# Kernel tuning notes

Hardware: AMD Instinct MI355X
Metric: run time of the kernel (lower is better)

The kernel has to match this reference:

```python
import jax, jax.numpy as jnp
from jax import lax
import numpy as np

EPS_START, EPS_END, EPS_DECAY = 1.0, 0.05, 10000.0


def gru_step(x, h, w_ih, w_hh, b_ih, b_hh):
    # PyTorch GRUCell math; gates stacked as [r, z, n]
    gi = x @ w_ih.T + b_ih
    gh = h @ w_hh.T + b_hh
    i_r, i_z, i_n = jnp.split(gi, 3, axis=1)
    h_r, h_z, h_n = jnp.split(gh, 3, axis=1)
    r = jax.nn.sigmoid(i_r + h_r)
    z = jax.nn.sigmoid(i_z + h_z)
    n = jnp.tanh(i_n + r * h_n)
    return (1.0 - z) * n + z * h


def setup_inputs() -> dict:
    key = jax.random.key(0)
    ks = jax.random.split(key, 7)
    V, E, H = 32000, 256, 512
    s = 0.05
    return {
        "embedding": jax.random.normal(ks[0], (V, E), jnp.float32) * s,
        "w_ih": jax.random.normal(ks[1], (3 * H, E), jnp.float32) * s,
        "w_hh": jax.random.normal(ks[2], (3 * H, H), jnp.float32) * s,
        "b_ih": jax.random.normal(ks[3], (3 * H,), jnp.float32) * s,
        "b_hh": jax.random.normal(ks[4], (3 * H,), jnp.float32) * s,
        "w_out": jax.random.normal(ks[5], (V, H), jnp.float32) * s,
        "b_out": jax.random.normal(ks[6], (V,), jnp.float32) * s,
        "seq_len": 256,
        "batch_size": 512,
    }


def reference(embedding, w_ih, w_hh, b_ih, b_hh, w_out, b_out, seq_len, batch_size):
    V, E = embedding.shape
    H = w_hh.shape[1]
    B = batch_size
    log_unif = jnp.float32(np.log(V))  # -log(vocab_size) fill for epsilon-greedy

    keys = jax.random.split(jax.random.key(42), seq_len)
    ts = jnp.arange(seq_len, dtype=jnp.float32)

    h0 = jnp.zeros((B, H), jnp.float32)
    x0 = jnp.broadcast_to(embedding[0], (B, E))  # start token id 0

    def step(carry, inp):
        h, x = carry
        t, k = inp
        k_eps, k_gum = jax.random.split(k)
        h = gru_step(x, h, w_ih, w_hh, b_ih, b_hh)
        logp = jax.nn.log_softmax(h @ w_out.T + b_out, axis=1)  # [B, V]
        eps_t = EPS_END + (EPS_START - EPS_END) * jnp.exp(-4.0 * t / EPS_DECAY)
        draw = eps_t >= jax.random.uniform(k_eps, (B,))
        masked = jnp.where(draw[:, None], -log_unif, logp)
        g = jax.random.gumbel(k_gum, (B, V), jnp.float32)
        sampled = jnp.argmax(masked + g, axis=1)  # [B] int
        lp = jnp.take_along_axis(logp, sampled[:, None], axis=1)[:, 0]
        x_next = embedding[sampled]
        return (h, x_next), (sampled, lp)

    _, (samples, lps) = lax.scan(step, (h0, x0), (ts, keys))
    return samples.T, lps.T  # [B, S] each
```

## Files before the change

### kernel.cpp

```cpp
#include <hip/hip_runtime.h>
#include <math.h>
#include <stdio.h>

#ifndef JAX_PARTITIONABLE
#define JAX_PARTITIONABLE 1
#endif

namespace {

constexpr int B  = 512;
constexpr int S  = 256;
constexpr int E  = 256;
constexpr int H  = 512;
constexpr int V  = 32000;
constexpr int G3 = 3 * H;
constexpr int VBLK = 64;
constexpr int BBLK = 256;
constexpr int NCH  = V / VBLK;
constexpr int NDMAX = 96;

typedef __bf16 bf16x8 __attribute__((ext_vector_type(8)));
typedef float  f32x4  __attribute__((ext_vector_type(4)));
typedef unsigned u32x4 __attribute__((ext_vector_type(4)));

__device__ __forceinline__ void tf2x32(unsigned k0, unsigned k1,
                                       unsigned x0, unsigned x1,
                                       unsigned& o0, unsigned& o1) {
  unsigned ks2 = k0 ^ k1 ^ 0x1BD11BDAu;
  x0 += k0; x1 += k1;
#define TFR(r) { x0 += x1; x1 = (x1 << (r)) | (x1 >> (32 - (r))); x1 ^= x0; }
  TFR(13) TFR(15) TFR(26) TFR(6)   x0 += k1;  x1 += ks2 + 1u;
  TFR(17) TFR(29) TFR(16) TFR(24)  x0 += ks2; x1 += k0 + 2u;
  TFR(13) TFR(15) TFR(26) TFR(6)   x0 += k0;  x1 += k1 + 3u;
  TFR(17) TFR(29) TFR(16) TFR(24)  x0 += k1;  x1 += ks2 + 4u;
  TFR(13) TFR(15) TFR(26) TFR(6)   x0 += ks2; x1 += k0 + 5u;
#undef TFR
  o0 = x0; o1 = x1;
}

__device__ __forceinline__ unsigned rbits(unsigned g0, unsigned g1,
                                          unsigned b, unsigned v) {
#if JAX_PARTITIONABLE
  unsigned y0, y1;
  tf2x32(g0, g1, 0u, b * (unsigned)V + v, y0, y1);
  return y0 ^ y1;
#else
  const unsigned N2 = (unsigned)(B/2) * (unsigned)V;
  unsigned ii = b * (unsigned)V + v;
  unsigned jj = (b < 256) ? ii : ii - N2;
  unsigned y0, y1;
  tf2x32(g0, g1, jj, N2 + jj, y0, y1);
  return (b < 256) ? y0 : y1;
#endif
}

__device__ __forceinline__ float u01_from_bits(unsigned bits) {
  return __uint_as_float(0x3f800000u | (bits >> 9)) - 1.0f;
}

__device__ __forceinline__ float gumbel_exact(unsigned bits) {
  float u = u01_from_bits(bits);
  if (u == 0.0f) u = 1.1754943508222875e-38f;
  float w = (float)(-log((double)u));
  return (float)(-log((double)w));
}

__device__ __forceinline__ float gumbel_fast(unsigned bits) {
  float u = u01_from_bits(bits);
  if (u == 0.0f) u = 1.1754943508222875e-38f;
  float w = -__logf(u);
  return -__logf(w);
}

__device__ __forceinline__ unsigned short f2bf(float f) {
  unsigned u = __float_as_uint(f);
  unsigned r = (u + 0x7fffu + ((u >> 16) & 1u)) >> 16;
  return (unsigned short)r;
}

__global__ void k_init_rng(unsigned* __restrict__ kq, unsigned* __restrict__ ke) {
  int t = threadIdx.x;
  unsigned h0, h1, e0, e1, g0, g1;
#if JAX_PARTITIONABLE
  tf2x32(0u, 42u, 0u, (unsigned)t, h0, h1);
  tf2x32(h0, h1, 0u, 0u, e0, e1);
  tf2x32(h0, h1, 0u, 1u, g0, g1);
#else
  unsigned a0, a1, b0, b1;
  if (t < 128) {
    tf2x32(0u, 42u, (unsigned)(2*t),   (unsigned)(256+2*t), a0, a1);
    tf2x32(0u, 42u, (unsigned)(2*t+1), (unsigned)(257+2*t), b0, b1);
    h0 = a0; h1 = b0;
  } else {
    int j = 2*t - 256;
    tf2x32(0u, 42u, (unsigned)j,     (unsigned)(256+j), a0, a1);
    tf2x32(0u, 42u, (unsigned)(j+1), (unsigned)(257+j), b0, b1);
    h0 = a1; h1 = b1;
  }
  unsigned p0, p1, q0, q1;
  tf2x32(h0, h1, 0u, 2u, p0, p1);
  tf2x32(h0, h1, 1u, 3u, q0, q1);
  e0 = p0; e1 = q0; g0 = p1; g1 = q1;
#endif
  ke[2*t] = e0; ke[2*t+1] = e1;
  kq[2*t] = g0; kq[2*t+1] = g1;
}

__global__ void k_init_draws(const unsigned* __restrict__ ke,
                             unsigned char* __restrict__ draws) {
  int t = blockIdx.x;
  int b = threadIdx.x;
  unsigned k0 = ke[2*t], k1 = ke[2*t+1];
  unsigned bits, y0, y1;
#if JAX_PARTITIONABLE
  tf2x32(k0, k1, 0u, (unsigned)b, y0, y1);
  bits = y0 ^ y1;
#else
  if (b < 256) { tf2x32(k0, k1, (unsigned)b,       (unsigned)(256+b), y0, y1); bits = y0; }
  else         { tf2x32(k0, k1, (unsigned)(b-256), (unsigned)b,       y0, y1); bits = y1; }
#endif
  float u   = u01_from_bits(bits);
  float tf  = (float)t;
  float ex  = expf(__fmul_rn(-4.0f, tf) / 10000.0f);
  float eps = __fadd_rn(0.05f, __fmul_rn(0.95f, ex));
  draws[t*B + b] = (eps >= u) ? 1 : 0;
}

__global__ void k_init_nd(const unsigned char* __restrict__ draws,
                          int* __restrict__ nd_slot) {
  int t = blockIdx.x;
  if (threadIdx.x != 0) return;
  int cnt = 0;
  for (int b = 0; b < B; b++) {
    if (!draws[t*B + b] && cnt < NDMAX) nd_slot[t*B + b] = cnt++;
    else nd_slot[t*B + b] = -1;
  }
}

__global__ __launch_bounds__(256) void k_pre_argmax(
    const unsigned* __restrict__ kq, const unsigned char* __restrict__ draws,
    int* __restrict__ pre) {
  const int job  = blockIdx.x * 4 + (threadIdx.x >> 6);
  const int lane = threadIdx.x & 63;
  const int t = job >> 9, b = job & (B - 1);
  if (!draws[t*B + b]) { if (lane == 0) pre[job] = -1; return; }
  const unsigned g0 = kq[2*t], g1 = kq[2*t+1];
  unsigned best = 0u; int bv = V;
  for (int v = lane; v < V; v += 64) {
    unsigned bits = rbits(g0, g1, (unsigned)b, (unsigned)v) >> 9;
    if (bits > best || (bits == best && v < bv)) { best = bits; bv = v; }
  }
#pragma unroll
  for (int m = 1; m < 64; m <<= 1) {
    unsigned ob = __shfl_xor(best, m, 64);
    int      ov = __shfl_xor(bv,   m, 64);
    if (ob > best || (ob == best && ov < bv)) { best = ob; bv = ov; }
  }
  if (lane == 0) pre[job] = bv;
}

__global__ void k_init_state(const float* __restrict__ emb,
                             float* __restrict__ x, float* __restrict__ h) {
  int b = blockIdx.x, tid = threadIdx.x;
  x[b*E + tid] = emb[tid];
  h[b*H + tid] = 0.0f;
  h[b*H + 256 + tid] = 0.0f;
}

__global__ void k_cast_w(const float* __restrict__ w,
                         unsigned short* __restrict__ wb) {
  int i = (blockIdx.x*256 + threadIdx.x) * 4;
#pragma unroll
  for (int j = 0; j < 4; j++) wb[i+j] = f2bf(w[i+j]);
}

__global__ __launch_bounds__(256) void k_gates(
    const float* __restrict__ x, const float* __restrict__ h,
    const float* __restrict__ w_ih, const float* __restrict__ w_hh,
    const float* __restrict__ b_ih, const float* __restrict__ b_hh,
    float* __restrict__ gi, float* __restrict__ gh) {
  const int z = blockIdx.z;
  const float* A    = z ? h    : x;
  const float* W    = z ? w_hh : w_ih;
  const float* bias = z ? b_hh : b_ih;
  float*       C    = z ? gh   : gi;
  const int K       = z ? H    : E;

  __shared__ __align__(16) float As[16][68];
  __shared__ __align__(16) float Ws[16][68];
  const int tid = threadIdx.x;
  const int tx = tid & 15, ty = tid >> 4;
  const int row0 = blockIdx.y * 64, col0 = blockIdx.x * 64;
  float acc[4][4] = {};
  for (int k0 = 0; k0 < K; k0 += 16) {
#pragma unroll
    for (int l = 0; l < 4; l++) {
      int idx = tid + l*256;
      int r = idx >> 4, kk = idx & 15;
      As[kk][r] = A[(row0 + r)*K + k0 + kk];
      Ws[kk][r] = W[(col0 + r)*K + k0 + kk];
    }
    __syncthreads();
#pragma unroll
    for (int kk = 0; kk < 16; kk++) {
      const float4 av = *(const float4*)&As[kk][ty*4];
      const float4 wv = *(const float4*)&Ws[kk][tx*4];
      const float a[4] = {av.x, av.y, av.z, av.w};
      const float w[4] = {wv.x, wv.y, wv.z, wv.w};
#pragma unroll
      for (int i = 0; i < 4; i++)
#pragma unroll
        for (int j = 0; j < 4; j++) acc[i][j] = fmaf(a[i], w[j], acc[i][j]);
    }
    __syncthreads();
  }
#pragma unroll
  for (int i = 0; i < 4; i++) {
    int r = row0 + ty*4 + i;
#pragma unroll
    for (int j = 0; j < 4; j++) {
      int c = col0 + tx*4 + j;
      C[r*G3 + c] = __fadd_rn(acc[i][j], bias[c]);
    }
  }
}

__device__ __forceinline__ float sigm_acc(float v) {
  return (float)(1.0 / (1.0 + exp(-(double)v)));
}
__device__ __forceinline__ float tanh_acc(float v) {
  return (float)tanh((double)v);
}

__global__ void k_gru_update(const float* __restrict__ gi,
                             const float* __restrict__ gh,
                             float* __restrict__ h,
                             unsigned short* __restrict__ h_bf) {
  int idx = blockIdx.x*256 + threadIdx.x;
  int b = idx >> 9, j = idx & 511;
  const float* gib = gi + b*G3;
  const float* ghb = gh + b*G3;
  float r  = sigm_acc(__fadd_rn(gib[j],     ghb[j]));
  float zz = sigm_acc(__fadd_rn(gib[H+j],   ghb[H+j]));
  float nn = tanh_acc(__fadd_rn(gib[2*H+j], __fmul_rn(r, ghb[2*H+j])));
  float hv = h[b*H + j];
  float t1 = __fmul_rn(__fsub_rn(1.0f, zz), nn);
  float t2 = __fmul_rn(zz, hv);
  float hn = __fadd_rn(t1, t2);
  h[idx] = hn;
  h_bf[idx] = f2bf(hn);
}

__global__ __launch_bounds__(256) void k_mfma_logits(
    const unsigned short* __restrict__ h_bf,
    const unsigned short* __restrict__ w_bf,
    const float* __restrict__ b_out,
    const unsigned* __restrict__ kq,
    const int* __restrict__ pre_t,
    const int* __restrict__ nd_slot_t,
    float* __restrict__ pmax, float* __restrict__ psum,
    float* __restrict__ plog,
    float* __restrict__ nd_keys, float* __restrict__ nd_kmax, int t) {
  const int vblk = blockIdx.x;
  const int bblk = blockIdx.y;
  const int tid  = threadIdx.x;
  const int lane = tid & 63, w = tid >> 6;
  const int quad = lane >> 4, l15 = lane & 15;

  __shared__ __align__(16) unsigned short hs[256*32];
  __shared__ __align__(16) unsigned short wt[64*32];

  f32x4 acc[4][4] = {};

  const int srow = tid >> 2;
  const int sk   = (tid & 3) * 8;
  const unsigned short* hA = h_bf + (size_t)(bblk*256 + srow)*H + sk;
  const unsigned short* wA = w_bf + (size_t)(vblk*64  + srow)*H + sk;

  u32x4 rh[4], rw;
#pragma unroll
  for (int rr = 0; rr < 4; rr++) rh[rr] = *(const u32x4*)(hA + rr*64*H);
  rw = *(const u32x4*)(wA);

  for (int k0 = 0; k0 < H; k0 += 32) {
    __syncthreads();
#pragma unroll
    for (int rr = 0; rr < 4; rr++)
      *(u32x4*)&hs[(rr*64 + srow)*32 + sk] = rh[rr];
    *(u32x4*)&wt[srow*32 + sk] = rw;
    __syncthreads();
    if (k0 + 32 < H) {
#pragma unroll
      for (int rr = 0; rr < 4; rr++) rh[rr] = *(const u32x4*)(hA + rr*64*H + k0 + 32);
      rw = *(const u32x4*)(wA + k0 + 32);
    }

    bf16x8 af[4], bfv[4];
#pragma unroll
    for (int mt = 0; mt < 4; mt++)
      af[mt] = __builtin_bit_cast(bf16x8,
          *(const u32x4*)&hs[(w*64 + mt*16 + l15)*32 + quad*8]);
#pragma unroll
    for (int nt = 0; nt < 4; nt++)
      bfv[nt] = __builtin_bit_cast(bf16x8,
          *(const u32x4*)&wt[(nt*16 + l15)*32 + quad*8]);
#pragma unroll
    for (int mt = 0; mt < 4; mt++)
#pragma unroll
      for (int nt = 0; nt < 4; nt++)
        acc[mt][nt] = __builtin_amdgcn_mfma_f32_16x16x32_bf16(
            af[mt], bfv[nt], acc[mt][nt], 0, 0, 0);
  }

  const int bW = bblk*256 + w*64;
  const int vW = vblk*64;
  const unsigned g0 = kq[2*t], g1 = kq[2*t+1];
  float bias[4];
#pragma unroll
  for (int nt = 0; nt < 4; nt++) bias[nt] = b_out[vW + nt*16 + l15];

#pragma unroll
  for (int mt = 0; mt < 4; mt++) {
#pragma unroll
    for (int r = 0; r < 4; r++) {
      const int b = bW + mt*16 + quad*4 + r;
      float lg[4];
#pragma unroll
      for (int nt = 0; nt < 4; nt++) lg[nt] = acc[mt][nt][r] + bias[nt];
      float lmax = fmaxf(fmaxf(lg[0], lg[1]), fmaxf(lg[2], lg[3]));
#pragma unroll
      for (int m = 1; m < 16; m <<= 1) lmax = fmaxf(lmax, __shfl_xor(lmax, m, 64));
      float ls = 0.0f;
#pragma unroll
      for (int nt = 0; nt < 4; nt++) ls += __expf(lg[nt] - lmax);
#pragma unroll
      for (int m = 1; m < 16; m <<= 1) ls += __shfl_xor(ls, m, 64);
      if (l15 == 0) { pmax[b*NCH + vblk] = lmax; psum[b*NCH + vblk] = ls; }
      const int pr = pre_t[b];
      if (pr >= 0) {
        int rel = pr - vW;
        if (rel >= 0 && rel < 64 && (rel & 15) == l15) plog[b] = lg[rel >> 4];
      } else {
        const int slot = nd_slot_t[b];
        if (slot >= 0) {
          float key[4];
#pragma unroll
          for (int nt = 0; nt < 4; nt++)
            key[nt] = lg[nt] + gumbel_fast(
                rbits(g0, g1, (unsigned)b, (unsigned)(vW + nt*16 + l15)));
          float* dst = nd_keys + (size_t)slot*V + vW + l15;
#pragma unroll
          for (int nt = 0; nt < 4; nt++) dst[nt*16] = key[nt];
          float kmx = fmaxf(fmaxf(key[0], key[1]), fmaxf(key[2], key[3]));
#pragma unroll
          for (int m = 1; m < 16; m <<= 1) kmx = fmaxf(kmx, __shfl_xor(kmx, m, 64));
          if (l15 == 0) nd_kmax[slot*NCH + vblk] = kmx;
        }
      }
    }
  }
}

__global__ __launch_bounds__(256) void k_finish(
    const float* __restrict__ pmax, const float* __restrict__ psum,
    const float* __restrict__ plog,
    const int* __restrict__ pre_t, const int* __restrict__ nd_slot_t,
    const float* __restrict__ nd_keys, const float* __restrict__ nd_kmax,
    const unsigned* __restrict__ kq,
    const float* __restrict__ h, const float* __restrict__ w_out,
    const float* __restrict__ b_out,
    const float* __restrict__ emb, float* __restrict__ x,
    float* __restrict__ out_samples, float* __restrict__ out_lps, int t) {
  const int b = blockIdx.x;
  const int tid = threadIdx.x;
  __shared__ float sA[256];
  __shared__ int   cand[160];
  __shared__ float cand_key[160], cand_lg[160];
  __shared__ int   ccnt;
  __shared__ int   s_samp;
  __shared__ float s_blog;

  float m = -INFINITY;
  for (int c = tid; c < NCH; c += 256) m = fmaxf(m, pmax[b*NCH + c]);
  sA[tid] = m; __syncthreads();
  for (int s = 128; s > 0; s >>= 1) {
    if (tid < s) sA[tid] = fmaxf(sA[tid], sA[tid+s]);
    __syncthreads();
  }
  const float M = sA[0];
  __syncthreads();
  float sum = 0.0f;
  for (int c = tid; c < NCH; c += 256)
    sum += psum[b*NCH + c] * expf(pmax[b*NCH + c] - M);
  sA[tid] = sum; __syncthreads();
  for (int s = 128; s > 0; s >>= 1) {
    if (tid < s) sA[tid] += sA[tid+s];
    __syncthreads();
  }
  const float SUM = sA[0];
  __syncthreads();

  const int pr = pre_t[b];
  if (pr >= 0) {
    if (tid == 0) { s_samp = pr; s_blog = plog[b]; }
  } else {
    const int slot = nd_slot_t[b];
    if (slot < 0) {
      if (tid == 0) { s_samp = 0; s_blog = plog[b]; }
    } else {
      const unsigned g0 = kq[2*t], g1 = kq[2*t+1];
      if (tid == 0) ccnt = 0;
      float km = -INFINITY;
      for (int c = tid; c < NCH; c += 256) km = fmaxf(km, nd_kmax[slot*NCH + c]);
      sA[tid] = km; __syncthreads();
      for (int s = 128; s > 0; s >>= 1) {
        if (tid < s) sA[tid] = fmaxf(sA[tid], sA[tid+s]);
        __syncthreads();
      }
      const float thr = sA[0] - 0.0859375f;
      __syncthreads();
      const float* keys = nd_keys + (size_t)slot*V;
      for (int c = tid; c < NCH; c += 256) {
        if (nd_kmax[slot*NCH + c] >= thr) {
          for (int j = 0; j < VBLK; j++) {
            float k = keys[c*VBLK + j];
            if (k >= thr) {
              int p = atomicAdd(&ccnt, 1);
              if (p < 160) cand[p] = c*VBLK + j;
            }
          }
        }
      }
      __syncthreads();
      const int nc = min(ccnt, 160);
      const int wid = tid >> 6, lane = tid & 63;
      for (int c = wid; c < nc; c += 4) {
        const int v = cand[c];
        const float* wr = w_out + (size_t)v*H;
        const float* hr = h + (size_t)b*H;
        float s = 0.0f;
#pragma unroll
        for (int i = 0; i < 8; i++) s = fmaf(hr[lane + 64*i], wr[lane + 64*i], s);
#pragma unroll
        for (int mm = 1; mm < 64; mm <<= 1) s += __shfl_xor(s, mm, 64);
        if (lane == 0) {
          float logit = __fadd_rn(s, b_out[v]);
          float key   = __fadd_rn(logit,
                          gumbel_exact(rbits(g0, g1, (unsigned)b, (unsigned)v)));
          cand_key[c] = key; cand_lg[c] = logit;
        }
      }
      __syncthreads();
      if (tid == 0) {
        float bk = -INFINITY; int bv = V; float bl = 0.0f;
        for (int c = 0; c < nc; c++) {
          float k = cand_key[c]; int v = cand[c];
          if (k > bk || (k == bk && v < bv)) { bk = k; bv = v; bl = cand_lg[c]; }
        }
        s_samp = bv; s_blog = bl;
      }
    }
  }
  __syncthreads();
  const int sampled = s_samp;
  if (tid == 0) {
    float lse = (float)log((double)SUM);
    float lp  = __fsub_rn(__fsub_rn(s_blog, M), lse);
    out_samples[b*S + t] = (float)sampled;
    out_lps[b*S + t]     = lp;
  }
  x[b*E + tid] = emb[sampled*E + tid];
}

}

extern "C" void kernel_launch(void* const* d_in, const int* in_sizes, int n_in,
                              void* d_out, int out_size, void* d_ws, size_t ws_size,
                              hipStream_t stream) {
  (void)in_sizes; (void)n_in; (void)out_size;
  const float* emb   = (const float*)d_in[0];
  const float* w_ih  = (const float*)d_in[1];
  const float* w_hh  = (const float*)d_in[2];
  const float* b_ih  = (const float*)d_in[3];
  const float* b_hh  = (const float*)d_in[4];
  const float* w_out = (const float*)d_in[5];
  const float* b_out = (const float*)d_in[6];
  float* out = (float*)d_out;

  char* wsb = (char*)d_ws;
  size_t off = 0;
  auto alloc = [&](size_t nbytes) {
    char* p = wsb + off;
    off += (nbytes + 255) & ~size_t(255);
    return p;
  };
  float* h     = (float*)alloc((size_t)B*H*4);
  float* x     = (float*)alloc((size_t)B*E*4);
  float* gi    = (float*)alloc((size_t)B*G3*4);
  float* gh    = (float*)alloc((size_t)B*G3*4);
  unsigned short* h_bf = (unsigned short*)alloc((size_t)B*H*2);
  unsigned short* w_bf = (unsigned short*)alloc((size_t)V*H*2);
  float* pmax  = (float*)alloc((size_t)B*NCH*4);
  float* psum  = (float*)alloc((size_t)B*NCH*4);
  float* plog  = (float*)alloc((size_t)B*4);
  unsigned* kq = (unsigned*)alloc((size_t)S*2*4);
  unsigned* ke = (unsigned*)alloc((size_t)S*2*4);
  unsigned char* draws = (unsigned char*)alloc((size_t)S*B);
  int* pre     = (int*)alloc((size_t)S*B*4);
  int* nd_slot = (int*)alloc((size_t)S*B*4);
  float* nd_keys = (float*)alloc((size_t)NDMAX*V*4);
  float* nd_kmax = (float*)alloc((size_t)NDMAX*NCH*4);
  if (off > ws_size) {
    fprintf(stderr, "kernel_launch: workspace too small (need %zu, have %zu)\n",
            off, ws_size);
    return;
  }

  k_init_rng<<<1, S, 0, stream>>>(kq, ke);
  k_init_draws<<<S, B, 0, stream>>>(ke, draws);
  k_init_nd<<<S, 64, 0, stream>>>(draws, nd_slot);
  k_pre_argmax<<<(S*B)/4, 256, 0, stream>>>(kq, draws, pre);
  k_init_state<<<B, 256, 0, stream>>>(emb, x, h);
  k_cast_w<<<(V*H)/1024, 256, 0, stream>>>(w_out, w_bf);

  for (int t = 0; t < S; t++) {
    k_gates<<<dim3(G3/64, B/64, 2), 256, 0, stream>>>(x, h, w_ih, w_hh,
                                                      b_ih, b_hh, gi, gh);
    k_gru_update<<<(B*H)/256, 256, 0, stream>>>(gi, gh, h, h_bf);
    k_mfma_logits<<<dim3(V/VBLK, B/BBLK), 256, 0, stream>>>(
        h_bf, w_bf, b_out, kq, pre + t*B, nd_slot + t*B,
        pmax, psum, plog, nd_keys, nd_kmax, t);
    k_finish<<<B, 256, 0, stream>>>(pmax, psum, plog, pre + t*B, nd_slot + t*B,
                                    nd_keys, nd_kmax, kq, h, w_out, b_out,
                                    emb, x, out, out + (size_t)B*S, t);
  }
}
```

Before: 37.23 ms.

## Pre-swizzle h and W_out into MFMA fragment layout, drop LDS staging

Writes bf16 h and the output weight directly into an MFMA-fragment-ordered layout, so each lane can load its 16-byte fragment straight from global memory. The logits kernel loses its shared-memory staging and the two barriers per k-step. The risk is that reuse now depends on L1/L2: each h fragment is read by 500 vblocks and each W fragment by 2 bblocks through cache. The GRU update kernel is also reworked so each thread handles 8 consecutive elements and writes a packed swizzled vector.

```diff
diff --git a/kernel.cpp b/kernel.cpp
--- a/kernel.cpp
+++ b/kernel.cpp
@@ -76,6 +76,11 @@
   unsigned u = __float_as_uint(f);
   unsigned r = (u + 0x7fffu + ((u >> 16) & 1u)) >> 16;
   return (unsigned short)r;
+}
+
+__device__ __forceinline__ size_t frag_off(int row, int k, int kTiles) {
+  return ((size_t)((row >> 4) * kTiles + (k >> 5)) * 64
+          + (row & 15) + 16 * ((k >> 3) & 3)) * 8 + (k & 7);
 }
 
 __global__ void k_init_rng(unsigned* __restrict__ kq, unsigned* __restrict__ ke) {
@@ -168,10 +173,15 @@
 }
 
 __global__ void k_cast_w(const float* __restrict__ w,
-                         unsigned short* __restrict__ wb) {
-  int i = (blockIdx.x*256 + threadIdx.x) * 4;
-#pragma unroll
-  for (int j = 0; j < 4; j++) wb[i+j] = f2bf(w[i+j]);
+                         unsigned short* __restrict__ w_sw) {
+  int g = blockIdx.x*256 + threadIdx.x;
+  int v  = g >> 6;
+  int k0 = (g & 63) * 8;
+  const float* src = w + (size_t)v*H + k0;
+  union { unsigned short s[8]; u32x4 vv; } u;
+#pragma unroll
+  for (int e = 0; e < 8; e++) u.s[e] = f2bf(src[e]);
+  *(u32x4*)&w_sw[frag_off(v, k0, H/32)] = u.vv;
 }
 
 __global__ __launch_bounds__(256) void k_gates(
@@ -235,25 +245,34 @@
 __global__ void k_gru_update(const float* __restrict__ gi,
                              const float* __restrict__ gh,
                              float* __restrict__ h,
-                             unsigned short* __restrict__ h_bf) {
-  int idx = blockIdx.x*256 + threadIdx.x;
-  int b = idx >> 9, j = idx & 511;
-  const float* gib = gi + b*G3;
-  const float* ghb = gh + b*G3;
-  float r  = sigm_acc(__fadd_rn(gib[j],     ghb[j]));
-  float zz = sigm_acc(__fadd_rn(gib[H+j],   ghb[H+j]));
-  float nn = tanh_acc(__fadd_rn(gib[2*H+j], __fmul_rn(r, ghb[2*H+j])));
-  float hv = h[b*H + j];
-  float t1 = __fmul_rn(__fsub_rn(1.0f, zz), nn);
-  float t2 = __fmul_rn(zz, hv);
-  float hn = __fadd_rn(t1, t2);
-  h[idx] = hn;
-  h_bf[idx] = f2bf(hn);
+                             unsigned short* __restrict__ h_sw) {
+  int g = blockIdx.x*256 + threadIdx.x;
+  int b  = g >> 6;
+  int j0 = (g & 63) * 8;
+  const float* gib = gi + (size_t)b*G3;
+  const float* ghb = gh + (size_t)b*G3;
+  float hn[8];
+  union { unsigned short s[8]; u32x4 vv; } u;
+#pragma unroll
+  for (int e = 0; e < 8; e++) {
+    int j = j0 + e;
+    float r  = sigm_acc(__fadd_rn(gib[j],     ghb[j]));
+    float zz = sigm_acc(__fadd_rn(gib[H+j],   ghb[H+j]));
+    float nn = tanh_acc(__fadd_rn(gib[2*H+j], __fmul_rn(r, ghb[2*H+j])));
+    float hv = h[(size_t)b*H + j];
+    float t1 = __fmul_rn(__fsub_rn(1.0f, zz), nn);
+    float t2 = __fmul_rn(zz, hv);
+    hn[e] = __fadd_rn(t1, t2);
+    u.s[e] = f2bf(hn[e]);
+  }
+#pragma unroll
+  for (int e = 0; e < 8; e++) h[(size_t)b*H + j0 + e] = hn[e];
+  *(u32x4*)&h_sw[frag_off(b, j0, H/32)] = u.vv;
 }
 
 __global__ __launch_bounds__(256) void k_mfma_logits(
-    const unsigned short* __restrict__ h_bf,
-    const unsigned short* __restrict__ w_bf,
+    const unsigned short* __restrict__ h_sw,
+    const unsigned short* __restrict__ w_sw,
     const float* __restrict__ b_out,
     const unsigned* __restrict__ kq,
     const int* __restrict__ pre_t,
@@ -267,43 +286,24 @@
   const int lane = tid & 63, w = tid >> 6;
   const int quad = lane >> 4, l15 = lane & 15;
 
-  __shared__ __align__(16) unsigned short hs[256*32];
-  __shared__ __align__(16) unsigned short wt[64*32];
-
   f32x4 acc[4][4] = {};
 
-  const int srow = tid >> 2;
-  const int sk   = (tid & 3) * 8;
-  const unsigned short* hA = h_bf + (size_t)(bblk*256 + srow)*H + sk;
-  const unsigned short* wA = w_bf + (size_t)(vblk*64  + srow)*H + sk;
-
-  u32x4 rh[4], rw;
-#pragma unroll
-  for (int rr = 0; rr < 4; rr++) rh[rr] = *(const u32x4*)(hA + rr*64*H);
-  rw = *(const u32x4*)(wA);
-
-  for (int k0 = 0; k0 < H; k0 += 32) {
-    __syncthreads();
-#pragma unroll
-    for (int rr = 0; rr < 4; rr++)
-      *(u32x4*)&hs[(rr*64 + srow)*32 + sk] = rh[rr];
-    *(u32x4*)&wt[srow*32 + sk] = rw;
-    __syncthreads();
-    if (k0 + 32 < H) {
-#pragma unroll
-      for (int rr = 0; rr < 4; rr++) rh[rr] = *(const u32x4*)(hA + rr*64*H + k0 + 32);
-      rw = *(const u32x4*)(wA + k0 + 32);
-    }
-
+  const int mtBase = bblk*16 + w*4;
+  const int ntBase = vblk*4;
+  const unsigned short* hp = h_sw + (size_t)mtBase*16*512 + lane*8;
+  const unsigned short* wp = w_sw + (size_t)ntBase*16*512 + lane*8;
+
+#pragma unroll 2
+  for (int kt = 0; kt < 16; kt++) {
     bf16x8 af[4], bfv[4];
 #pragma unroll
     for (int mt = 0; mt < 4; mt++)
       af[mt] = __builtin_bit_cast(bf16x8,
-          *(const u32x4*)&hs[(w*64 + mt*16 + l15)*32 + quad*8]);
+          *(const u32x4*)(hp + (size_t)(mt*16 + kt)*512));
 #pragma unroll
     for (int nt = 0; nt < 4; nt++)
       bfv[nt] = __builtin_bit_cast(bf16x8,
-          *(const u32x4*)&wt[(nt*16 + l15)*32 + quad*8]);
+          *(const u32x4*)(wp + (size_t)(nt*16 + kt)*512));
 #pragma unroll
     for (int mt = 0; mt < 4; mt++)
 #pragma unroll
@@ -498,8 +498,8 @@
   float* x     = (float*)alloc((size_t)B*E*4);
   float* gi    = (float*)alloc((size_t)B*G3*4);
   float* gh    = (float*)alloc((size_t)B*G3*4);
-  unsigned short* h_bf = (unsigned short*)alloc((size_t)B*H*2);
-  unsigned short* w_bf = (unsigned short*)alloc((size_t)V*H*2);
+  unsigned short* h_sw = (unsigned short*)alloc((size_t)B*H*2);
+  unsigned short* w_sw = (unsigned short*)alloc((size_t)V*H*2);
   float* pmax  = (float*)alloc((size_t)B*NCH*4);
   float* psum  = (float*)alloc((size_t)B*NCH*4);
   float* plog  = (float*)alloc((size_t)B*4);
@@ -521,14 +521,14 @@
   k_init_nd<<<S, 64, 0, stream>>>(draws, nd_slot);
   k_pre_argmax<<<(S*B)/4, 256, 0, stream>>>(kq, draws, pre);
   k_init_state<<<B, 256, 0, stream>>>(emb, x, h);
-  k_cast_w<<<(V*H)/1024, 256, 0, stream>>>(w_out, w_bf);
+  k_cast_w<<<(V*H/8)/256, 256, 0, stream>>>(w_out, w_sw);
 
   for (int t = 0; t < S; t++) {
     k_gates<<<dim3(G3/64, B/64, 2), 256, 0, stream>>>(x, h, w_ih, w_hh,
                                                       b_ih, b_hh, gi, gh);
-    k_gru_update<<<(B*H)/256, 256, 0, stream>>>(gi, gh, h, h_bf);
+    k_gru_update<<<(B*H/8)/256, 256, 0, stream>>>(gi, gh, h, h_sw);
     k_mfma_logits<<<dim3(V/VBLK, B/BBLK), 256, 0, stream>>>(
-        h_bf, w_bf, b_out, kq, pre + t*B, nd_slot + t*B,
+        h_sw, w_sw, b_out, kq, pre + t*B, nd_slot + t*B,
         pmax, psum, plog, nd_keys, nd_kmax, t);
     k_finish<<<B, 256, 0, stream>>>(pmax, psum, plog, pre + t*B, nd_slot + t*B,
                                     nd_keys, nd_kmax, kq, h, w_out, b_out,
```

After: 41.94 ms. 12.7% more time.
